# Kernel tuning notes

Measured on AMD Instinct MI355X. Metric: run time of the kernel, lower is better.

The kernel has to match this reference:

```python
import jax, jax.numpy as jnp
import numpy as np

EPS = 1e-5  # torch LayerNorm default

def _ln(x):
    # LayerNorm over last dim, no affine (elementwise_affine=False)
    m = jnp.mean(x, axis=-1, keepdims=True)
    v = jnp.var(x, axis=-1, keepdims=True)
    return (x - m) / jnp.sqrt(v + EPS)

def _build_orthogonal(phi):
    """Orthogonal matrix of the 'X' RBS circuit on d qubits (unary subspace).
    phi has 2d-3 angles: a descending diagonal of d-1 adjacent Givens rotations
    followed by an ascending diagonal of d-2. Each RBS(theta) acts on coords
    (k, k+1) as [[cos, sin], [-sin, cos]]."""
    d = (phi.shape[0] + 3) // 2
    W = jnp.eye(d, dtype=phi.dtype)
    wires = list(range(d - 1)) + list(range(d - 3, -1, -1))  # 2d-3 gates
    for g, k in enumerate(wires):
        c, s = jnp.cos(phi[g]), jnp.sin(phi[g])
        rk, rk1 = W[k], W[k + 1]
        W = W.at[k].set(c * rk + s * rk1)
        W = W.at[k + 1].set(-s * rk + c * rk1)
    return W

def setup_inputs() -> dict:
    key = jax.random.key(0)
    ks = jax.random.split(key, 8)
    B, N, E, H, dh = 16, 1024, 512, 8, 64
    return {
        "x": jax.random.normal(ks[0], (B, N, E), jnp.float32),
        "Wv": jax.random.normal(ks[1], (H, dh, dh), jnp.float32) / np.sqrt(dh).astype(np.float32),
        "bv": jnp.zeros((H, dh), jnp.float32),
        "phi": jax.random.uniform(ks[2], (H, 2 * dh - 3), jnp.float32, 0.0, 2.0 * np.pi),
        "W1": jax.random.normal(ks[3], (E, E), jnp.float32) / np.sqrt(E).astype(np.float32),
        "b1": jnp.zeros((E,), jnp.float32),
        "W2": jax.random.normal(ks[4], (E, E), jnp.float32) / np.sqrt(E).astype(np.float32),
        "b2": jnp.zeros((E,), jnp.float32),
    }

def reference(x, Wv, bv, phi, W1, b1, W2, b2):
    B, N, E = x.shape
    H = Wv.shape[0]
    dh = E // H
    xn = _ln(x)                                    # norm1
    xh = xn.reshape(B, N, H, dh)                   # per-head slices
    Worth = jax.vmap(_build_orthogonal)(phi)       # [H, dh, dh]
    # per-head value projection (nn.Linear weights stored as [in, out])
    V = jnp.einsum('bnhd,hde->bnhe', xh, Wv) + bv  # [B,N,H,dh]
    # quantum attention scores: loader(x_j) -> W(phi) -> inverse loader(x_i),
    # rescaled by |x_i||x_j|  ==  A_ij = x_i^T W(phi) x_j
    A = jnp.einsum('bnhd,hde,bmhe->bhnm', xh, Worth, xh)
    P = jax.nn.softmax(A / np.float32(np.sqrt(dh)), axis=-1)
    attn = jnp.einsum('bhnm,bmhe->bnhe', P, V)
    head_out = _ln(attn + xh)                      # per-head LN over dh
    res = head_out.reshape(B, N, E) + x            # MHA + residual
    # merger: Linear -> GELU(exact) -> Linear on norm2(res)
    h = jax.nn.gelu(_ln(res) @ W1 + b1, approximate=False) @ W2 + b2
    return h + res
```

## Files before the change

kernel.cpp:

```cpp
#include <hip/hip_runtime.h>
#include <hip/hip_bf16.h>
#include <math.h>

#define B_  16
#define N_  1024
#define E_  512
#define H_  8

typedef __attribute__((ext_vector_type(8)))  __bf16 bf16x8;
typedef __attribute__((ext_vector_type(4)))  float  f32x4;
typedef __attribute__((ext_vector_type(16))) float  f32x16;
typedef __attribute__((ext_vector_type(4)))  unsigned int u32x4;

struct alignas(16) bf8pack { __hip_bfloat16 v[8]; };
struct alignas(8)  bf4pack { __hip_bfloat16 v[4]; };

static __device__ __forceinline__ float bf2f(__hip_bfloat16 x) { return __bfloat162float(x); }
static __device__ __forceinline__ __hip_bfloat16 f2bf(float x) { return __float2bfloat16(x); }

static __device__ __forceinline__ unsigned pkbf(float lo, float hi) {
    unsigned r;
    asm("v_cvt_pk_bf16_f32 %0, %1, %2" : "=v"(r) : "v"(lo), "v"(hi));
    return r;
}
static __device__ __forceinline__ void swap32(unsigned &a, unsigned &b) {
    asm("v_permlane32_swap_b32 %0, %1" : "+v"(a), "+v"(b));
}
static __device__ __forceinline__ void gload16(const __hip_bfloat16* g, __hip_bfloat16* l) {
    __builtin_amdgcn_global_load_lds(
        (const __attribute__((address_space(1))) unsigned*)g,
        (__attribute__((address_space(3))) unsigned*)l, 16, 0, 0);
}
#define MFMA32(a, b, c) __builtin_amdgcn_mfma_f32_32x32x16_bf16((a), (b), (c), 0, 0, 0)
#define MFMA16(a, b, c) __builtin_amdgcn_mfma_f32_16x16x32_bf16((a), (b), (c), 0, 0, 0)

static __device__ __forceinline__ float gelu_f(float v) {
    float z = fabsf(v) * 0.70710678118654752f;
    float t = 1.0f / fmaf(0.3275911f, z, 1.0f);
    float p = t * fmaf(t, fmaf(t, fmaf(t, fmaf(t, 1.061405429f, -1.453152027f),
                                       1.421413741f), -0.284496736f), 0.254829592f);
    float e = __builtin_amdgcn_exp2f(-z * z * 1.4426950408889634f);
    float erf = 1.0f - p * e;
    erf = copysignf(erf, v);
    return 0.5f * v * (1.0f + erf);
}

__global__ __launch_bounds__(64) void k_worth(const float* __restrict__ phi,
                                              const float* __restrict__ Wv,
                                              __hip_bfloat16* __restrict__ worth_t,
                                              __hip_bfloat16* __restrict__ wvt) {
    const float SCL = 0.18033688011112042f;
    __shared__ float W[64 * 65];
    int h = blockIdx.x;
    int t = threadIdx.x;
    for (int i = 0; i < 64; ++i) W[i * 65 + t] = (i == t) ? 1.0f : 0.0f;
    for (int g = 0; g < 125; ++g) {
        int k = (g < 63) ? g : (124 - g);
        float ph = phi[h * 125 + g];
        float c = cosf(ph), s = sinf(ph);
        float a  = W[k * 65 + t];
        float b  = W[(k + 1) * 65 + t];
        W[k * 65 + t]       =  c * a + s * b;
        W[(k + 1) * 65 + t] = -s * a + c * b;
    }
    for (int d = 0; d < 64; ++d)
        worth_t[h * 4096 + t * 64 + d] = f2bf(W[d * 65 + t] * SCL);
    for (int d = 0; d < 64; ++d)
        wvt[h * 4096 + t * 64 + d] = f2bf(Wv[h * 4096 + d * 64 + t]);
}

__global__ __launch_bounds__(256) void k_transpose(const float* __restrict__ W1,
                                                   const float* __restrict__ W2,
                                                   __hip_bfloat16* __restrict__ w1t,
                                                   __hip_bfloat16* __restrict__ w2t) {
    const float* src = blockIdx.y ? W2 : W1;
    __hip_bfloat16* dst = blockIdx.y ? w2t : w1t;
    int i0 = (blockIdx.x & 7) * 64, o0 = (blockIdx.x >> 3) * 64;
    int tid = threadIdx.x;
    __shared__ float ts[64][65];
    int r = tid >> 4, c4 = (tid & 15) * 4;
#pragma unroll
    for (int j4 = 0; j4 < 4; ++j4) {
        float4 v = *reinterpret_cast<const float4*>(&src[(size_t)(i0 + r + 16 * j4) * 512 + o0 + c4]);
        ts[r + 16 * j4][c4 + 0] = v.x; ts[r + 16 * j4][c4 + 1] = v.y;
        ts[r + 16 * j4][c4 + 2] = v.z; ts[r + 16 * j4][c4 + 3] = v.w;
    }
    __syncthreads();
    int o = tid >> 3, cg = tid & 7;
#pragma unroll
    for (int half = 0; half < 2; ++half) {
        int oo = o + 32 * half;
        bf8pack p;
#pragma unroll
        for (int j = 0; j < 8; ++j) p.v[j] = f2bf(ts[cg * 8 + j][oo]);
        *reinterpret_cast<bf8pack*>(&dst[(size_t)(o0 + oo) * 512 + i0 + cg * 8]) = p;
    }
}

template <typename T>
__global__ __launch_bounds__(256) void k_ln(const T* __restrict__ in,
                                            __hip_bfloat16* __restrict__ out) {
    int w = threadIdx.x >> 6, l = threadIdx.x & 63;
    size_t row = (size_t)blockIdx.x * 4 + w;
    float vv[8];
    if constexpr (sizeof(T) == 4) {
        const float* p = (const float*)in + row * 512 + l * 8;
        float4 v0 = *reinterpret_cast<const float4*>(p);
        float4 v1 = *reinterpret_cast<const float4*>(p + 4);
        vv[0]=v0.x; vv[1]=v0.y; vv[2]=v0.z; vv[3]=v0.w;
        vv[4]=v1.x; vv[5]=v1.y; vv[6]=v1.z; vv[7]=v1.w;
    } else {
        const __hip_bfloat16* p = (const __hip_bfloat16*)in + row * 512 + l * 8;
        bf16x8 u = *reinterpret_cast<const bf16x8*>(p);
#pragma unroll
        for (int j = 0; j < 8; ++j) vv[j] = (float)u[j];
    }
    float s = 0.f, sq = 0.f;
#pragma unroll
    for (int j = 0; j < 8; ++j) { s += vv[j]; sq += vv[j] * vv[j]; }
#pragma unroll
    for (int o = 32; o >= 1; o >>= 1) { s += __shfl_xor(s, o); sq += __shfl_xor(sq, o); }
    float mean = s * (1.0f / 512.0f);
    float var  = sq * (1.0f / 512.0f) - mean * mean;
    float rstd = rsqrtf(var + 1e-5f);
    bf8pack ob;
#pragma unroll
    for (int j = 0; j < 8; ++j) ob.v[j] = f2bf((vv[j] - mean) * rstd);
    *reinterpret_cast<bf8pack*>(out + row * 512 + l * 8) = ob;
}

__global__ __launch_bounds__(256) void k_proj(const __hip_bfloat16* __restrict__ xn,
                                              const __hip_bfloat16* __restrict__ worth_t,
                                              const __hip_bfloat16* __restrict__ wvt,
                                              const float* __restrict__ bv,
                                              __hip_bfloat16* __restrict__ xw,
                                              __hip_bfloat16* __restrict__ vt) {
    int h = blockIdx.y, rt = blockIdx.x;
    int tid = threadIdx.x, w = tid >> 6, l = tid & 63;
    int lr = l & 15, lg = l >> 4;
    int nw = rt * 64 + w * 16;
    int b  = (rt * 64) >> 10;
    int n0 = (rt * 64) & 1023;
    size_t bh = (size_t)b * H_ + h;

    const __hip_bfloat16* xp = xn + (size_t)(nw + lr) * 512 + h * 64 + lg * 8;
    bf16x8 xf0 = *reinterpret_cast<const bf16x8*>(xp);
    bf16x8 xf1 = *reinterpret_cast<const bf16x8*>(xp + 32);

    f32x4 accw[4] = {}, accv[4] = {};
#pragma unroll
    for (int g = 0; g < 4; ++g) {
        const __hip_bfloat16* wp = worth_t + h * 4096 + (g * 16 + lr) * 64 + lg * 8;
        accw[g] = MFMA16(*reinterpret_cast<const bf16x8*>(wp), xf0, accw[g]);
        accw[g] = MFMA16(*reinterpret_cast<const bf16x8*>(wp + 32), xf1, accw[g]);
        const __hip_bfloat16* vp = wvt + h * 4096 + (g * 16 + lr) * 64 + lg * 8;
        accv[g] = MFMA16(xf0, *reinterpret_cast<const bf16x8*>(vp), accv[g]);
        accv[g] = MFMA16(xf1, *reinterpret_cast<const bf16x8*>(vp + 32), accv[g]);
    }
#pragma unroll
    for (int g = 0; g < 4; ++g) {
        bf4pack pw;
#pragma unroll
        for (int r = 0; r < 4; ++r) pw.v[r] = f2bf(accw[g][r]);
        *reinterpret_cast<bf4pack*>(xw + (bh * N_ + n0 + w * 16 + lr) * 64 + g * 16 + lg * 4) = pw;
        float bb = bv[h * 64 + g * 16 + lr];
        bf4pack pv;
#pragma unroll
        for (int r = 0; r < 4; ++r) pv.v[r] = f2bf(accv[g][r] + bb);
        *reinterpret_cast<bf4pack*>(vt + (bh * 64 + g * 16 + lr) * N_ + n0 + w * 16 + lg * 4) = pv;
    }
}

__global__ __launch_bounds__(512, 4) void k_attn(const __hip_bfloat16* __restrict__ xn,
                                                 const __hip_bfloat16* __restrict__ xw,
                                                 const __hip_bfloat16* __restrict__ vt,
                                                 const float* __restrict__ x,
                                                 __hip_bfloat16* __restrict__ res) {
    int h = blockIdx.x, b = blockIdx.z;
    int tid = threadIdx.x;
    int w = tid >> 6, l = tid & 63;
    int lq = l & 31, hi = l >> 5;
    int q0 = blockIdx.y * 256 + w * 32;
    size_t bh = (size_t)b * H_ + h;

    __shared__ __hip_bfloat16 kb[2][128 * 64];
    __shared__ __hip_bfloat16 vb[2][64 * 128];
    __shared__ float lred[8][32];

    int krow = w * 16 + (l >> 3);
    const __hip_bfloat16* ksrc = xn + ((size_t)b * N_ + krow) * 512 + h * 64
                               + (((l & 7) ^ (krow & 7)) << 3);
    int vrow0 = w * 8 + (l >> 4);
    int vrow1 = vrow0 + 4;
    const __hip_bfloat16* vsrc0 = vt + (bh * 64 + vrow0) * N_ + (((l & 15) ^ (vrow0 & 15)) << 3);
    const __hip_bfloat16* vsrc1 = vt + (bh * 64 + vrow1) * N_ + (((l & 15) ^ (vrow1 & 15)) << 3);

#define STAGE(t) do { int bf_ = (t) & 1; \
        gload16(ksrc + (size_t)((t) * 128) * 512,     &kb[bf_][(w * 16) * 64]); \
        gload16(ksrc + (size_t)((t) * 128 + 8) * 512, &kb[bf_][(w * 16 + 8) * 64]); \
        gload16(vsrc0 + (t) * 128, &vb[bf_][(w * 8) * 128]); \
        gload16(vsrc1 + (t) * 128, &vb[bf_][(w * 8 + 4) * 128]); } while (0)
#define TILE_BAR() do { \
        asm volatile("s_waitcnt vmcnt(0)" ::: "memory"); \
        __builtin_amdgcn_s_barrier(); \
        __builtin_amdgcn_sched_barrier(0); } while (0)

    const __hip_bfloat16* qp = xw + (bh * N_ + q0 + lq) * 64 + 8 * hi;
    bf16x8 qf0 = *reinterpret_cast<const bf16x8*>(qp);
    bf16x8 qf1 = *reinterpret_cast<const bf16x8*>(qp + 16);
    bf16x8 qf2 = *reinterpret_cast<const bf16x8*>(qp + 32);
    bf16x8 qf3 = *reinterpret_cast<const bf16x8*>(qp + 48);

    f32x16 o0 = {}, o1 = {};
    float l_run = 0.f;
    int kso = lq & 7;
    int vso = lq & 15;

    auto body = [&](int bf_, int mm) {
        const __hip_bfloat16* kc = &kb[bf_][mm * 64 * 64];
        const __hip_bfloat16* vc = &vb[bf_][0];
        f32x16 s0 = {}, s1 = {};
        __builtin_amdgcn_s_setprio(1);
#pragma unroll
        for (int kd = 0; kd < 4; ++kd) {
            bf16x8 qf = (kd == 0) ? qf0 : (kd == 1) ? qf1 : (kd == 2) ? qf2 : qf3;
            int sl = ((kd * 2 + hi) ^ kso) << 3;
            bf16x8 ka0 = *reinterpret_cast<const bf16x8*>(kc + lq * 64 + sl);
            bf16x8 ka1 = *reinterpret_cast<const bf16x8*>(kc + (lq + 32) * 64 + sl);
            s0 = MFMA32(ka0, qf, s0);
            s1 = MFMA32(ka1, qf, s1);
        }
        __builtin_amdgcn_s_setprio(0);
#pragma unroll
        for (int i = 0; i < 16; ++i) {
            s0[i] = __builtin_amdgcn_exp2f(s0[i]);
            s1[i] = __builtin_amdgcn_exp2f(s1[i]);
        }
        float ls = 0.f;
#pragma unroll
        for (int i = 0; i < 16; ++i) ls += s0[i] + s1[i];
        l_run += ls;
        bf16x8 pa[4];
        {
            unsigned u0 = pkbf(s0[0], s0[1]), u1 = pkbf(s0[2], s0[3]);
            unsigned u2 = pkbf(s0[4], s0[5]), u3 = pkbf(s0[6], s0[7]);
            swap32(u0, u2); swap32(u1, u3);
            u32x4 uu = {u0, u1, u2, u3};
            pa[0] = __builtin_bit_cast(bf16x8, uu);
        }
        {
            unsigned u0 = pkbf(s0[8], s0[9]),   u1 = pkbf(s0[10], s0[11]);
            unsigned u2 = pkbf(s0[12], s0[13]), u3 = pkbf(s0[14], s0[15]);
            swap32(u0, u2); swap32(u1, u3);
            u32x4 uu = {u0, u1, u2, u3};
            pa[1] = __builtin_bit_cast(bf16x8, uu);
        }
        {
            unsigned u0 = pkbf(s1[0], s1[1]), u1 = pkbf(s1[2], s1[3]);
            unsigned u2 = pkbf(s1[4], s1[5]), u3 = pkbf(s1[6], s1[7]);
            swap32(u0, u2); swap32(u1, u3);
            u32x4 uu = {u0, u1, u2, u3};
            pa[2] = __builtin_bit_cast(bf16x8, uu);
        }
        {
            unsigned u0 = pkbf(s1[8], s1[9]),   u1 = pkbf(s1[10], s1[11]);
            unsigned u2 = pkbf(s1[12], s1[13]), u3 = pkbf(s1[14], s1[15]);
            swap32(u0, u2); swap32(u1, u3);
            u32x4 uu = {u0, u1, u2, u3};
            pa[3] = __builtin_bit_cast(bf16x8, uu);
        }
        __builtin_amdgcn_s_setprio(1);
#pragma unroll
        for (int ks = 0; ks < 4; ++ks) {
            int sl = ((mm * 8 + ks * 2 + hi) ^ vso) << 3;
            bf16x8 v0 = *reinterpret_cast<const bf16x8*>(vc + lq * 128 + sl);
            bf16x8 v1 = *reinterpret_cast<const bf16x8*>(vc + (lq + 32) * 128 + sl);
            o0 = MFMA32(pa[ks], v0, o0);
            o1 = MFMA32(pa[ks], v1, o1);
        }
        __builtin_amdgcn_s_setprio(0);
    };

    STAGE(0);
    TILE_BAR();
    for (int t = 0; t < 7; ++t) {
        STAGE(t + 1);
        body(t & 1, 0);
        body(t & 1, 1);
        TILE_BAR();
    }
    body(1, 0);
    body(1, 1);

    float lt = l_run + __shfl_xor(l_run, 32);
    if (hi == 0) lred[w][lq] = 1.0f / lt;
#pragma unroll
    for (int r = 0; r < 16; ++r) {
        int qr = (r & 3) + 8 * (r >> 2) + 4 * hi;
        float li = lred[w][qr];
        size_t base = ((size_t)b * N_ + q0 + qr) * 512 + h * 64;
        float t0 = o0[r] * li + bf2f(xn[base + lq]);
        float t1 = o1[r] * li + bf2f(xn[base + 32 + lq]);
        float s1v = t0 + t1, s2v = t0 * t0 + t1 * t1;
#pragma unroll
        for (int off = 16; off >= 1; off >>= 1) { s1v += __shfl_xor(s1v, off); s2v += __shfl_xor(s2v, off); }
        float mean = s1v * (1.0f / 64.0f);
        float var  = s2v * (1.0f / 64.0f) - mean * mean;
        float rstd = rsqrtf(var + 1e-5f);
        res[base + lq]      = f2bf((t0 - mean) * rstd + x[base + lq]);
        res[base + 32 + lq] = f2bf((t1 - mean) * rstd + x[base + 32 + lq]);
    }
#undef STAGE
#undef TILE_BAR
}

template <int MODE>
__global__ __launch_bounds__(256, 5) void k_gemm(const __hip_bfloat16* __restrict__ A,
                                                 const __hip_bfloat16* __restrict__ Bt,
                                                 const float* __restrict__ bias,
                                                 const __hip_bfloat16* __restrict__ resid,
                                                 __hip_bfloat16* __restrict__ outb,
                                                 float* __restrict__ outf) {
    int m0 = blockIdx.x * 128, nn0 = blockIdx.y * 64;
    int tid = threadIdx.x, w = tid >> 6, l = tid & 63;
    int lr = l & 15, lg = l >> 4;
    __shared__ __hip_bfloat16 bs[2][64 * 128];

    int srow = w * 16 + (l >> 4);
    int sslot = l & 15;

#define GSTAGE(c) do { \
        _Pragma("unroll") \
        for (int i_ = 0; i_ < 4; ++i_) { \
            int row_ = srow + i_ * 4; \
            gload16(Bt + (size_t)(nn0 + row_) * 512 + (c) * 128 + ((sslot ^ (row_ & 15)) << 3), \
                    &bs[(c) & 1][(w * 16 + i_ * 4) * 128]); \
        } } while (0)

    GSTAGE(0);
    asm volatile("s_waitcnt vmcnt(0)" ::: "memory");
    __builtin_amdgcn_s_barrier();
    __builtin_amdgcn_sched_barrier(0);

    f32x4 acc0[4] = {}, acc1[4] = {};
    const __hip_bfloat16* ap0 = A + (size_t)(m0 + w * 32 + lr) * 512 + lg * 8;
    const __hip_bfloat16* ap1 = ap0 + 16 * 512;
#pragma unroll
    for (int c = 0; c < 4; ++c) {
        if (c < 3) GSTAGE(c + 1);
        const __hip_bfloat16* bc = &bs[c & 1][0];
#pragma unroll
        for (int kk = 0; kk < 4; ++kk) {
            bf16x8 a0 = *reinterpret_cast<const bf16x8*>(ap0 + c * 128 + kk * 32);
            bf16x8 a1 = *reinterpret_cast<const bf16x8*>(ap1 + c * 128 + kk * 32);
#pragma unroll
            for (int g = 0; g < 4; ++g) {
                int row = g * 16 + lr;
                bf16x8 bf = *reinterpret_cast<const bf16x8*>(
                    bc + row * 128 + (((kk * 4 + lg) ^ (row & 15)) << 3));
                acc0[g] = MFMA16(a0, bf, acc0[g]);
                acc1[g] = MFMA16(a1, bf, acc1[g]);
            }
        }
        if (c < 3) {
            asm volatile("s_waitcnt vmcnt(0)" ::: "memory");
            __builtin_amdgcn_s_barrier();
            __builtin_amdgcn_sched_barrier(0);
        }
    }
#undef GSTAGE
#pragma unroll
    for (int g = 0; g < 4; ++g) {
        int col = nn0 + g * 16 + lr;
        float bb = bias[col];
#pragma unroll
        for (int r = 0; r < 4; ++r) {
            int row0 = m0 + w * 32 + lg * 4 + r;
            float v0 = acc0[g][r] + bb;
            float v1 = acc1[g][r] + bb;
            if (MODE == 0) {
                outb[(size_t)row0 * 512 + col] = f2bf(gelu_f(v0));
                outb[(size_t)(row0 + 16) * 512 + col] = f2bf(gelu_f(v1));
            } else {
                size_t i0 = (size_t)row0 * 512 + col;
                size_t i1 = (size_t)(row0 + 16) * 512 + col;
                outf[i0] = v0 + bf2f(resid[i0]);
                outf[i1] = v1 + bf2f(resid[i1]);
            }
        }
    }
}

extern "C" void kernel_launch(void* const* d_in, const int* in_sizes, int n_in,
                              void* d_out, int out_size, void* d_ws, size_t ws_size,
                              hipStream_t stream) {
    const float* x   = (const float*)d_in[0];
    const float* Wv  = (const float*)d_in[1];
    const float* bv  = (const float*)d_in[2];
    const float* phi = (const float*)d_in[3];
    const float* W1  = (const float*)d_in[4];
    const float* b1  = (const float*)d_in[5];
    const float* W2  = (const float*)d_in[6];
    const float* b2  = (const float*)d_in[7];
    float* out = (float*)d_out;

    char* ws = (char*)d_ws;
    __hip_bfloat16* worth_t = (__hip_bfloat16*)(ws + 0);
    __hip_bfloat16* wvt     = (__hip_bfloat16*)(ws + 65536);
    __hip_bfloat16* w1t     = (__hip_bfloat16*)(ws + 131072);
    __hip_bfloat16* w2t     = (__hip_bfloat16*)(ws + 655360);
    __hip_bfloat16* xn      = (__hip_bfloat16*)(ws + 1179648);
    __hip_bfloat16* xw      = (__hip_bfloat16*)(ws + 17956864);
    __hip_bfloat16* vt      = (__hip_bfloat16*)(ws + 34734080);
    __hip_bfloat16* res     = (__hip_bfloat16*)(ws + 51511296);
    __hip_bfloat16* xn2     = (__hip_bfloat16*)(ws + 68288512);
    __hip_bfloat16* y1      = (__hip_bfloat16*)(ws + 85065728);

    k_worth<<<dim3(8), dim3(64), 0, stream>>>(phi, Wv, worth_t, wvt);
    k_transpose<<<dim3(64, 2), dim3(256), 0, stream>>>(W1, W2, w1t, w2t);
    k_ln<float><<<dim3(4096), dim3(256), 0, stream>>>(x, xn);
    k_proj<<<dim3(256, 8), dim3(256), 0, stream>>>(xn, worth_t, wvt, bv, xw, vt);
    k_attn<<<dim3(8, 4, 16), dim3(512), 0, stream>>>(xn, xw, vt, x, res);
    k_ln<__hip_bfloat16><<<dim3(4096), dim3(256), 0, stream>>>(res, xn2);
    k_gemm<0><<<dim3(128, 8), dim3(256), 0, stream>>>(xn2, w1t, b1, nullptr, y1, nullptr);
    k_gemm<1><<<dim3(128, 8), dim3(256), 0, stream>>>(y1, w2t, b2, res, nullptr, out);
}
```

Measured before the change: 179.4 us.

## Software-pipeline attention over 64-key tiles, merge prep kernels, read bf16 residual

Attention now processes 64-key tiles with a triple-buffered K and quad-buffered V ring. QK^T of the next tile overlaps with PV of the previous tile, and the barrier waits with vmcnt(2) so loads stay in flight. The two weight-prep kernels are merged into one launch, which saves a launch. The first LayerNorm also writes a bf16 copy of x so attention reads a half-size residual instead of fp32. That copy costs extra writes and adds bf16 rounding to the residual, and more LDS use may limit occupancy.

```diff
diff --git a/kernel.cpp b/kernel.cpp
--- a/kernel.cpp
+++ b/kernel.cpp
@@ -45,61 +45,67 @@
     return 0.5f * v * (1.0f + erf);
 }
 
-__global__ __launch_bounds__(64) void k_worth(const float* __restrict__ phi,
+__global__ __launch_bounds__(256) void k_prep(const float* __restrict__ phi,
                                               const float* __restrict__ Wv,
+                                              const float* __restrict__ W1,
+                                              const float* __restrict__ W2,
                                               __hip_bfloat16* __restrict__ worth_t,
-                                              __hip_bfloat16* __restrict__ wvt) {
-    const float SCL = 0.18033688011112042f;
-    __shared__ float W[64 * 65];
-    int h = blockIdx.x;
-    int t = threadIdx.x;
-    for (int i = 0; i < 64; ++i) W[i * 65 + t] = (i == t) ? 1.0f : 0.0f;
-    for (int g = 0; g < 125; ++g) {
-        int k = (g < 63) ? g : (124 - g);
-        float ph = phi[h * 125 + g];
-        float c = cosf(ph), s = sinf(ph);
-        float a  = W[k * 65 + t];
-        float b  = W[(k + 1) * 65 + t];
-        W[k * 65 + t]       =  c * a + s * b;
-        W[(k + 1) * 65 + t] = -s * a + c * b;
-    }
-    for (int d = 0; d < 64; ++d)
-        worth_t[h * 4096 + t * 64 + d] = f2bf(W[d * 65 + t] * SCL);
-    for (int d = 0; d < 64; ++d)
-        wvt[h * 4096 + t * 64 + d] = f2bf(Wv[h * 4096 + d * 64 + t]);
-}
-
-__global__ __launch_bounds__(256) void k_transpose(const float* __restrict__ W1,
-                                                   const float* __restrict__ W2,
-                                                   __hip_bfloat16* __restrict__ w1t,
-                                                   __hip_bfloat16* __restrict__ w2t) {
-    const float* src = blockIdx.y ? W2 : W1;
-    __hip_bfloat16* dst = blockIdx.y ? w2t : w1t;
-    int i0 = (blockIdx.x & 7) * 64, o0 = (blockIdx.x >> 3) * 64;
+                                              __hip_bfloat16* __restrict__ wvt,
+                                              __hip_bfloat16* __restrict__ w1t,
+                                              __hip_bfloat16* __restrict__ w2t) {
+    __shared__ float sh[64 * 65];
     int tid = threadIdx.x;
-    __shared__ float ts[64][65];
-    int r = tid >> 4, c4 = (tid & 15) * 4;
-#pragma unroll
-    for (int j4 = 0; j4 < 4; ++j4) {
-        float4 v = *reinterpret_cast<const float4*>(&src[(size_t)(i0 + r + 16 * j4) * 512 + o0 + c4]);
-        ts[r + 16 * j4][c4 + 0] = v.x; ts[r + 16 * j4][c4 + 1] = v.y;
-        ts[r + 16 * j4][c4 + 2] = v.z; ts[r + 16 * j4][c4 + 3] = v.w;
-    }
-    __syncthreads();
-    int o = tid >> 3, cg = tid & 7;
-#pragma unroll
-    for (int half = 0; half < 2; ++half) {
-        int oo = o + 32 * half;
-        bf8pack p;
-#pragma unroll
-        for (int j = 0; j < 8; ++j) p.v[j] = f2bf(ts[cg * 8 + j][oo]);
-        *reinterpret_cast<bf8pack*>(&dst[(size_t)(o0 + oo) * 512 + i0 + cg * 8]) = p;
-    }
-}
-
-template <typename T>
+    if (blockIdx.x < 128) {
+        int bid = blockIdx.x;
+        const float* src = (bid & 1) ? W2 : W1;
+        __hip_bfloat16* dst = (bid & 1) ? w2t : w1t;
+        int tile = bid >> 1;
+        int i0 = (tile & 7) * 64, o0 = (tile >> 3) * 64;
+        float (*ts)[65] = (float(*)[65])sh;
+        int r = tid >> 4, c4 = (tid & 15) * 4;
+#pragma unroll
+        for (int j4 = 0; j4 < 4; ++j4) {
+            float4 v = *reinterpret_cast<const float4*>(&src[(size_t)(i0 + r + 16 * j4) * 512 + o0 + c4]);
+            ts[r + 16 * j4][c4 + 0] = v.x; ts[r + 16 * j4][c4 + 1] = v.y;
+            ts[r + 16 * j4][c4 + 2] = v.z; ts[r + 16 * j4][c4 + 3] = v.w;
+        }
+        __syncthreads();
+        int o = tid >> 3, cg = tid & 7;
+#pragma unroll
+        for (int half = 0; half < 2; ++half) {
+            int oo = o + 32 * half;
+            bf8pack p;
+#pragma unroll
+            for (int j = 0; j < 8; ++j) p.v[j] = f2bf(ts[cg * 8 + j][oo]);
+            *reinterpret_cast<bf8pack*>(&dst[(size_t)(o0 + oo) * 512 + i0 + cg * 8]) = p;
+        }
+    } else {
+        const float SCL = 0.18033688011112042f;
+        int h = blockIdx.x - 128;
+        int t = tid;
+        if (t < 64) {
+            for (int i = 0; i < 64; ++i) sh[i * 65 + t] = (i == t) ? 1.0f : 0.0f;
+            for (int g = 0; g < 125; ++g) {
+                int k = (g < 63) ? g : (124 - g);
+                float ph = phi[h * 125 + g];
+                float c = cosf(ph), s = sinf(ph);
+                float a  = sh[k * 65 + t];
+                float b  = sh[(k + 1) * 65 + t];
+                sh[k * 65 + t]       =  c * a + s * b;
+                sh[(k + 1) * 65 + t] = -s * a + c * b;
+            }
+            for (int d = 0; d < 64; ++d)
+                worth_t[h * 4096 + t * 64 + d] = f2bf(sh[d * 65 + t] * SCL);
+            for (int d = 0; d < 64; ++d)
+                wvt[h * 4096 + t * 64 + d] = f2bf(Wv[h * 4096 + d * 64 + t]);
+        }
+    }
+}
+
+template <typename T, bool WX>
 __global__ __launch_bounds__(256) void k_ln(const T* __restrict__ in,
-                                            __hip_bfloat16* __restrict__ out) {
+                                            __hip_bfloat16* __restrict__ out,
+                                            __hip_bfloat16* __restrict__ outx) {
     int w = threadIdx.x >> 6, l = threadIdx.x & 63;
     size_t row = (size_t)blockIdx.x * 4 + w;
     float vv[8];
@@ -114,6 +120,12 @@
         bf16x8 u = *reinterpret_cast<const bf16x8*>(p);
 #pragma unroll
         for (int j = 0; j < 8; ++j) vv[j] = (float)u[j];
+    }
+    if constexpr (WX) {
+        bf8pack xo;
+#pragma unroll
+        for (int j = 0; j < 8; ++j) xo.v[j] = f2bf(vv[j]);
+        *reinterpret_cast<bf8pack*>(outx + row * 512 + l * 8) = xo;
     }
     float s = 0.f, sq = 0.f;
 #pragma unroll
@@ -174,34 +186,30 @@
 __global__ __launch_bounds__(512, 4) void k_attn(const __hip_bfloat16* __restrict__ xn,
                                                  const __hip_bfloat16* __restrict__ xw,
                                                  const __hip_bfloat16* __restrict__ vt,
-                                                 const float* __restrict__ x,
+                                                 const __hip_bfloat16* __restrict__ xb,
                                                  __hip_bfloat16* __restrict__ res) {
     int h = blockIdx.x, b = blockIdx.z;
     int tid = threadIdx.x;
     int w = tid >> 6, l = tid & 63;
     int lq = l & 31, hi = l >> 5;
+    int so = lq & 7;
     int q0 = blockIdx.y * 256 + w * 32;
     size_t bh = (size_t)b * H_ + h;
 
-    __shared__ __hip_bfloat16 kb[2][128 * 64];
-    __shared__ __hip_bfloat16 vb[2][64 * 128];
+    __shared__ __hip_bfloat16 kb[3][4096];
+    __shared__ __hip_bfloat16 vb[4][4096];
     __shared__ float lred[8][32];
 
-    int krow = w * 16 + (l >> 3);
-    const __hip_bfloat16* ksrc = xn + ((size_t)b * N_ + krow) * 512 + h * 64
-                               + (((l & 7) ^ (krow & 7)) << 3);
-    int vrow0 = w * 8 + (l >> 4);
-    int vrow1 = vrow0 + 4;
-    const __hip_bfloat16* vsrc0 = vt + (bh * 64 + vrow0) * N_ + (((l & 15) ^ (vrow0 & 15)) << 3);
-    const __hip_bfloat16* vsrc1 = vt + (bh * 64 + vrow1) * N_ + (((l & 15) ^ (vrow1 & 15)) << 3);
-
-#define STAGE(t) do { int bf_ = (t) & 1; \
-        gload16(ksrc + (size_t)((t) * 128) * 512,     &kb[bf_][(w * 16) * 64]); \
-        gload16(ksrc + (size_t)((t) * 128 + 8) * 512, &kb[bf_][(w * 16 + 8) * 64]); \
-        gload16(vsrc0 + (t) * 128, &vb[bf_][(w * 8) * 128]); \
-        gload16(vsrc1 + (t) * 128, &vb[bf_][(w * 8 + 4) * 128]); } while (0)
-#define TILE_BAR() do { \
-        asm volatile("s_waitcnt vmcnt(0)" ::: "memory"); \
+    int rloc = w * 8 + (l >> 3);
+    int gs = ((l & 7) ^ (rloc & 7)) << 3;
+    const __hip_bfloat16* ksrc = xn + ((size_t)b * N_ + rloc) * 512 + h * 64 + gs;
+    const __hip_bfloat16* vsrc = vt + (bh * 64 + rloc) * N_ + gs;
+
+#define STAGE(t) do { \
+        gload16(ksrc + (size_t)(t) * 64 * 512, &kb[(t) % 3][w * 512]); \
+        gload16(vsrc + (t) * 64, &vb[(t) & 3][w * 512]); } while (0)
+#define TILE_BAR(nvm) do { \
+        asm volatile("s_waitcnt vmcnt(" #nvm ")" ::: "memory"); \
         __builtin_amdgcn_s_barrier(); \
         __builtin_amdgcn_sched_barrier(0); } while (0)
 
@@ -213,24 +221,38 @@
 
     f32x16 o0 = {}, o1 = {};
     float l_run = 0.f;
-    int kso = lq & 7;
-    int vso = lq & 15;
-
-    auto body = [&](int bf_, int mm) {
-        const __hip_bfloat16* kc = &kb[bf_][mm * 64 * 64];
-        const __hip_bfloat16* vc = &vb[bf_][0];
-        f32x16 s0 = {}, s1 = {};
+    f32x16 s0, s1;
+    bf16x8 paA[4], paB[4];
+
+    auto qk = [&](int t) {
+        const __hip_bfloat16* kc = &kb[t % 3][0];
+        s0 = (f32x16){}; s1 = (f32x16){};
         __builtin_amdgcn_s_setprio(1);
 #pragma unroll
         for (int kd = 0; kd < 4; ++kd) {
             bf16x8 qf = (kd == 0) ? qf0 : (kd == 1) ? qf1 : (kd == 2) ? qf2 : qf3;
-            int sl = ((kd * 2 + hi) ^ kso) << 3;
+            int sl = ((kd * 2 + hi) ^ so) << 3;
             bf16x8 ka0 = *reinterpret_cast<const bf16x8*>(kc + lq * 64 + sl);
             bf16x8 ka1 = *reinterpret_cast<const bf16x8*>(kc + (lq + 32) * 64 + sl);
             s0 = MFMA32(ka0, qf, s0);
             s1 = MFMA32(ka1, qf, s1);
         }
         __builtin_amdgcn_s_setprio(0);
+    };
+    auto pv = [&](int t, const bf16x8* pa) {
+        const __hip_bfloat16* vc = &vb[t & 3][0];
+        __builtin_amdgcn_s_setprio(1);
+#pragma unroll
+        for (int ks = 0; ks < 4; ++ks) {
+            int sl = ((ks * 2 + hi) ^ so) << 3;
+            bf16x8 v0 = *reinterpret_cast<const bf16x8*>(vc + lq * 64 + sl);
+            bf16x8 v1 = *reinterpret_cast<const bf16x8*>(vc + (lq + 32) * 64 + sl);
+            o0 = MFMA32(pa[ks], v0, o0);
+            o1 = MFMA32(pa[ks], v1, o1);
+        }
+        __builtin_amdgcn_s_setprio(0);
+    };
+    auto exppack = [&](bf16x8* pa) {
 #pragma unroll
         for (int i = 0; i < 16; ++i) {
             s0[i] = __builtin_amdgcn_exp2f(s0[i]);
@@ -240,7 +262,6 @@
 #pragma unroll
         for (int i = 0; i < 16; ++i) ls += s0[i] + s1[i];
         l_run += ls;
-        bf16x8 pa[4];
         {
             unsigned u0 = pkbf(s0[0], s0[1]), u1 = pkbf(s0[2], s0[3]);
             unsigned u2 = pkbf(s0[4], s0[5]), u3 = pkbf(s0[6], s0[7]);
@@ -269,28 +290,34 @@
             u32x4 uu = {u0, u1, u2, u3};
             pa[3] = __builtin_bit_cast(bf16x8, uu);
         }
-        __builtin_amdgcn_s_setprio(1);
-#pragma unroll
-        for (int ks = 0; ks < 4; ++ks) {
-            int sl = ((mm * 8 + ks * 2 + hi) ^ vso) << 3;
-            bf16x8 v0 = *reinterpret_cast<const bf16x8*>(vc + lq * 128 + sl);
-            bf16x8 v1 = *reinterpret_cast<const bf16x8*>(vc + (lq + 32) * 128 + sl);
-            o0 = MFMA32(pa[ks], v0, o0);
-            o1 = MFMA32(pa[ks], v1, o1);
-        }
-        __builtin_amdgcn_s_setprio(0);
     };
 
-    STAGE(0);
-    TILE_BAR();
-    for (int t = 0; t < 7; ++t) {
-        STAGE(t + 1);
-        body(t & 1, 0);
-        body(t & 1, 1);
-        TILE_BAR();
-    }
-    body(1, 0);
-    body(1, 1);
+    STAGE(0); STAGE(1);
+    TILE_BAR(2);
+    STAGE(2);
+    qk(0); exppack(paA);
+    TILE_BAR(2);
+
+    for (int tp = 0; tp < 6; ++tp) {
+        int t = 2 * tp + 1;
+        STAGE(t + 2);
+        qk(t);
+        pv(t - 1, paA);
+        exppack(paB);
+        TILE_BAR(2);
+        STAGE(t + 3);
+        qk(t + 1);
+        pv(t, paB);
+        exppack(paA);
+        TILE_BAR(2);
+    }
+    STAGE(15);
+    qk(13); pv(12, paA); exppack(paB);
+    TILE_BAR(2);
+    qk(14); pv(13, paB); exppack(paA);
+    TILE_BAR(0);
+    qk(15); pv(14, paA); exppack(paB);
+    pv(15, paB);
 
     float lt = l_run + __shfl_xor(l_run, 32);
     if (hi == 0) lred[w][lq] = 1.0f / lt;
@@ -307,8 +334,8 @@
         float mean = s1v * (1.0f / 64.0f);
         float var  = s2v * (1.0f / 64.0f) - mean * mean;
         float rstd = rsqrtf(var + 1e-5f);
-        res[base + lq]      = f2bf((t0 - mean) * rstd + x[base + lq]);
-        res[base + 32 + lq] = f2bf((t1 - mean) * rstd + x[base + 32 + lq]);
+        res[base + lq]      = f2bf((t0 - mean) * rstd + bf2f(xb[base + lq]));
+        res[base + 32 + lq] = f2bf((t1 - mean) * rstd + bf2f(xb[base + 32 + lq]));
     }
 #undef STAGE
 #undef TILE_BAR
@@ -415,13 +442,13 @@
     __hip_bfloat16* res     = (__hip_bfloat16*)(ws + 51511296);
     __hip_bfloat16* xn2     = (__hip_bfloat16*)(ws + 68288512);
     __hip_bfloat16* y1      = (__hip_bfloat16*)(ws + 85065728);
-
-    k_worth<<<dim3(8), dim3(64), 0, stream>>>(phi, Wv, worth_t, wvt);
-    k_transpose<<<dim3(64, 2), dim3(256), 0, stream>>>(W1, W2, w1t, w2t);
-    k_ln<float><<<dim3(4096), dim3(256), 0, stream>>>(x, xn);
+    __hip_bfloat16* xb      = (__hip_bfloat16*)(ws + 101842944);
+
+    k_prep<<<dim3(136), dim3(256), 0, stream>>>(phi, Wv, W1, W2, worth_t, wvt, w1t, w2t);
+    k_ln<float, true><<<dim3(4096), dim3(256), 0, stream>>>(x, xn, xb);
     k_proj<<<dim3(256, 8), dim3(256), 0, stream>>>(xn, worth_t, wvt, bv, xw, vt);
-    k_attn<<<dim3(8, 4, 16), dim3(512), 0, stream>>>(xn, xw, vt, x, res);
-    k_ln<__hip_bfloat16><<<dim3(4096), dim3(256), 0, stream>>>(res, xn2);
+    k_attn<<<dim3(8, 4, 16), dim3(512), 0, stream>>>(xn, xw, vt, xb, res);
+    k_ln<__hip_bfloat16, false><<<dim3(4096), dim3(256), 0, stream>>>(res, xn2, nullptr);
     k_gemm<0><<<dim3(128, 8), dim3(256), 0, stream>>>(xn2, w1t, b1, nullptr, y1, nullptr);
     k_gemm<1><<<dim3(128, 8), dim3(256), 0, stream>>>(y1, w2t, b2, res, nullptr, out);
 }
```

After: 186.0 us. 1.04x slower.

## Fold LayerNorm2 into GEMM1 epilogue via row stats and weight column sums

Applied to the files above, without the earlier changes.

Replaces the second LayerNorm kernel, which wrote a normalized bf16 copy of res, with a small row-statistics kernel. GEMM1 now runs directly on res and applies rstd*(acc) - mean*rstd*colsum(W1) + b1 in its epilogue. It also merges the weight prep kernels into one launch, stages the proj outputs through LDS for coalesced stores, and passes a bf16 copy of x to attention instead of fp32. The cost is precision: GEMM1 multiplies un-centered bf16 res values, while the column sums are fp32 over the unrounded W1 rather than the bf16 w1t the GEMM uses, so the mean correction no longer cancels exactly.

```diff
diff --git a/kernel.cpp b/kernel.cpp
--- a/kernel.cpp
+++ b/kernel.cpp
@@ -45,76 +45,82 @@
     return 0.5f * v * (1.0f + erf);
 }
 
-__global__ __launch_bounds__(64) void k_worth(const float* __restrict__ phi,
+__global__ __launch_bounds__(256) void k_prep(const float* __restrict__ phi,
                                               const float* __restrict__ Wv,
+                                              const float* __restrict__ W1,
+                                              const float* __restrict__ W2,
                                               __hip_bfloat16* __restrict__ worth_t,
-                                              __hip_bfloat16* __restrict__ wvt) {
-    const float SCL = 0.18033688011112042f;
-    __shared__ float W[64 * 65];
-    int h = blockIdx.x;
-    int t = threadIdx.x;
-    for (int i = 0; i < 64; ++i) W[i * 65 + t] = (i == t) ? 1.0f : 0.0f;
-    for (int g = 0; g < 125; ++g) {
-        int k = (g < 63) ? g : (124 - g);
-        float ph = phi[h * 125 + g];
-        float c = cosf(ph), s = sinf(ph);
-        float a  = W[k * 65 + t];
-        float b  = W[(k + 1) * 65 + t];
-        W[k * 65 + t]       =  c * a + s * b;
-        W[(k + 1) * 65 + t] = -s * a + c * b;
-    }
-    for (int d = 0; d < 64; ++d)
-        worth_t[h * 4096 + t * 64 + d] = f2bf(W[d * 65 + t] * SCL);
-    for (int d = 0; d < 64; ++d)
-        wvt[h * 4096 + t * 64 + d] = f2bf(Wv[h * 4096 + d * 64 + t]);
-}
-
-__global__ __launch_bounds__(256) void k_transpose(const float* __restrict__ W1,
-                                                   const float* __restrict__ W2,
-                                                   __hip_bfloat16* __restrict__ w1t,
-                                                   __hip_bfloat16* __restrict__ w2t) {
-    const float* src = blockIdx.y ? W2 : W1;
-    __hip_bfloat16* dst = blockIdx.y ? w2t : w1t;
-    int i0 = (blockIdx.x & 7) * 64, o0 = (blockIdx.x >> 3) * 64;
+                                              __hip_bfloat16* __restrict__ wvt,
+                                              __hip_bfloat16* __restrict__ w1t,
+                                              __hip_bfloat16* __restrict__ w2t,
+                                              float* __restrict__ csum1) {
+    __shared__ float sh[64 * 65];
     int tid = threadIdx.x;
-    __shared__ float ts[64][65];
-    int r = tid >> 4, c4 = (tid & 15) * 4;
-#pragma unroll
-    for (int j4 = 0; j4 < 4; ++j4) {
-        float4 v = *reinterpret_cast<const float4*>(&src[(size_t)(i0 + r + 16 * j4) * 512 + o0 + c4]);
-        ts[r + 16 * j4][c4 + 0] = v.x; ts[r + 16 * j4][c4 + 1] = v.y;
-        ts[r + 16 * j4][c4 + 2] = v.z; ts[r + 16 * j4][c4 + 3] = v.w;
-    }
-    __syncthreads();
-    int o = tid >> 3, cg = tid & 7;
-#pragma unroll
-    for (int half = 0; half < 2; ++half) {
-        int oo = o + 32 * half;
-        bf8pack p;
-#pragma unroll
-        for (int j = 0; j < 8; ++j) p.v[j] = f2bf(ts[cg * 8 + j][oo]);
-        *reinterpret_cast<bf8pack*>(&dst[(size_t)(o0 + oo) * 512 + i0 + cg * 8]) = p;
-    }
-}
-
-template <typename T>
-__global__ __launch_bounds__(256) void k_ln(const T* __restrict__ in,
-                                            __hip_bfloat16* __restrict__ out) {
+    if (blockIdx.x < 128) {
+        int bid = blockIdx.x;
+        const float* src = (bid & 1) ? W2 : W1;
+        __hip_bfloat16* dst = (bid & 1) ? w2t : w1t;
+        int tile = bid >> 1;
+        int i0 = (tile & 7) * 64, o0 = (tile >> 3) * 64;
+        float (*ts)[65] = (float(*)[65])sh;
+        int r = tid >> 4, c4 = (tid & 15) * 4;
+#pragma unroll
+        for (int j4 = 0; j4 < 4; ++j4) {
+            float4 v = *reinterpret_cast<const float4*>(&src[(size_t)(i0 + r + 16 * j4) * 512 + o0 + c4]);
+            ts[r + 16 * j4][c4 + 0] = v.x; ts[r + 16 * j4][c4 + 1] = v.y;
+            ts[r + 16 * j4][c4 + 2] = v.z; ts[r + 16 * j4][c4 + 3] = v.w;
+        }
+        __syncthreads();
+        int o = tid >> 3, cg = tid & 7;
+#pragma unroll
+        for (int half = 0; half < 2; ++half) {
+            int oo = o + 32 * half;
+            bf8pack p;
+#pragma unroll
+            for (int j = 0; j < 8; ++j) p.v[j] = f2bf(ts[cg * 8 + j][oo]);
+            *reinterpret_cast<bf8pack*>(&dst[(size_t)(o0 + oo) * 512 + i0 + cg * 8]) = p;
+        }
+    } else if (blockIdx.x < 136) {
+        const float SCL = 0.18033688011112042f;
+        int h = blockIdx.x - 128;
+        int t = tid;
+        if (t < 64) {
+            for (int i = 0; i < 64; ++i) sh[i * 65 + t] = (i == t) ? 1.0f : 0.0f;
+            for (int g = 0; g < 125; ++g) {
+                int k = (g < 63) ? g : (124 - g);
+                float ph = phi[h * 125 + g];
+                float c = cosf(ph), s = sinf(ph);
+                float a  = sh[k * 65 + t];
+                float b  = sh[(k + 1) * 65 + t];
+                sh[k * 65 + t]       =  c * a + s * b;
+                sh[(k + 1) * 65 + t] = -s * a + c * b;
+            }
+            for (int d = 0; d < 64; ++d)
+                worth_t[h * 4096 + t * 64 + d] = f2bf(sh[d * 65 + t] * SCL);
+            for (int d = 0; d < 64; ++d)
+                wvt[h * 4096 + t * 64 + d] = f2bf(Wv[h * 4096 + d * 64 + t]);
+        }
+    } else {
+        int o = (blockIdx.x - 136) * 256 + tid;
+        float s = 0.f;
+        for (int i = 0; i < 512; ++i) s += W1[(size_t)i * 512 + o];
+        csum1[o] = s;
+    }
+}
+
+__global__ __launch_bounds__(256) void k_ln1(const float* __restrict__ in,
+                                             __hip_bfloat16* __restrict__ out,
+                                             __hip_bfloat16* __restrict__ outx) {
     int w = threadIdx.x >> 6, l = threadIdx.x & 63;
     size_t row = (size_t)blockIdx.x * 4 + w;
-    float vv[8];
-    if constexpr (sizeof(T) == 4) {
-        const float* p = (const float*)in + row * 512 + l * 8;
-        float4 v0 = *reinterpret_cast<const float4*>(p);
-        float4 v1 = *reinterpret_cast<const float4*>(p + 4);
-        vv[0]=v0.x; vv[1]=v0.y; vv[2]=v0.z; vv[3]=v0.w;
-        vv[4]=v1.x; vv[5]=v1.y; vv[6]=v1.z; vv[7]=v1.w;
-    } else {
-        const __hip_bfloat16* p = (const __hip_bfloat16*)in + row * 512 + l * 8;
-        bf16x8 u = *reinterpret_cast<const bf16x8*>(p);
-#pragma unroll
-        for (int j = 0; j < 8; ++j) vv[j] = (float)u[j];
-    }
+    const float* p = in + row * 512 + l * 8;
+    float4 v0 = *reinterpret_cast<const float4*>(p);
+    float4 v1 = *reinterpret_cast<const float4*>(p + 4);
+    float vv[8] = {v0.x, v0.y, v0.z, v0.w, v1.x, v1.y, v1.z, v1.w};
+    bf8pack xo;
+#pragma unroll
+    for (int j = 0; j < 8; ++j) xo.v[j] = f2bf(vv[j]);
+    *reinterpret_cast<bf8pack*>(outx + row * 512 + l * 8) = xo;
     float s = 0.f, sq = 0.f;
 #pragma unroll
     for (int j = 0; j < 8; ++j) { s += vv[j]; sq += vv[j] * vv[j]; }
@@ -127,6 +133,22 @@
 #pragma unroll
     for (int j = 0; j < 8; ++j) ob.v[j] = f2bf((vv[j] - mean) * rstd);
     *reinterpret_cast<bf8pack*>(out + row * 512 + l * 8) = ob;
+}
+
+__global__ __launch_bounds__(256) void k_rowstat(const __hip_bfloat16* __restrict__ res,
+                                                 float2* __restrict__ rs) {
+    int w = threadIdx.x >> 6, l = threadIdx.x & 63;
+    size_t row = (size_t)blockIdx.x * 4 + w;
+    bf16x8 u = *reinterpret_cast<const bf16x8*>(res + row * 512 + l * 8);
+    float s = 0.f, sq = 0.f;
+#pragma unroll
+    for (int j = 0; j < 8; ++j) { float a = (float)u[j]; s += a; sq = fmaf(a, a, sq); }
+#pragma unroll
+    for (int o = 32; o >= 1; o >>= 1) { s += __shfl_xor(s, o); sq += __shfl_xor(sq, o); }
+    float mean = s * (1.0f / 512.0f);
+    float var  = sq * (1.0f / 512.0f) - mean * mean;
+    float rstd = rsqrtf(var + 1e-5f);
+    if (l == 0) rs[row] = make_float2(rstd, mean * rstd);
 }
 
 __global__ __launch_bounds__(256) void k_proj(const __hip_bfloat16* __restrict__ xn,
@@ -143,6 +165,9 @@
     int n0 = (rt * 64) & 1023;
     size_t bh = (size_t)b * H_ + h;
 
+    __shared__ __hip_bfloat16 xw_l[64 * 72];
+    __shared__ __hip_bfloat16 vt_l[64 * 72];
+
     const __hip_bfloat16* xp = xn + (size_t)(nw + lr) * 512 + h * 64 + lg * 8;
     bf16x8 xf0 = *reinterpret_cast<const bf16x8*>(xp);
     bf16x8 xf1 = *reinterpret_cast<const bf16x8*>(xp + 32);
@@ -162,19 +187,33 @@
         bf4pack pw;
 #pragma unroll
         for (int r = 0; r < 4; ++r) pw.v[r] = f2bf(accw[g][r]);
-        *reinterpret_cast<bf4pack*>(xw + (bh * N_ + n0 + w * 16 + lr) * 64 + g * 16 + lg * 4) = pw;
+        *reinterpret_cast<bf4pack*>(&xw_l[(w * 16 + lr) * 72 + g * 16 + lg * 4]) = pw;
         float bb = bv[h * 64 + g * 16 + lr];
         bf4pack pv;
 #pragma unroll
         for (int r = 0; r < 4; ++r) pv.v[r] = f2bf(accv[g][r] + bb);
-        *reinterpret_cast<bf4pack*>(vt + (bh * 64 + g * 16 + lr) * N_ + n0 + w * 16 + lg * 4) = pv;
+        *reinterpret_cast<bf4pack*>(&vt_l[(g * 16 + lr) * 72 + w * 16 + lg * 4]) = pv;
+    }
+    __syncthreads();
+    {
+        int rr = tid >> 2, c0 = (tid & 3) * 16;
+        bf8pack p0 = *reinterpret_cast<const bf8pack*>(&xw_l[rr * 72 + c0]);
+        bf8pack p1 = *reinterpret_cast<const bf8pack*>(&xw_l[rr * 72 + c0 + 8]);
+        __hip_bfloat16* d1 = xw + (bh * N_ + n0 + rr) * 64 + c0;
+        *reinterpret_cast<bf8pack*>(d1)     = p0;
+        *reinterpret_cast<bf8pack*>(d1 + 8) = p1;
+        bf8pack q0 = *reinterpret_cast<const bf8pack*>(&vt_l[rr * 72 + c0]);
+        bf8pack q1 = *reinterpret_cast<const bf8pack*>(&vt_l[rr * 72 + c0 + 8]);
+        __hip_bfloat16* d2 = vt + (bh * 64 + rr) * N_ + n0 + c0;
+        *reinterpret_cast<bf8pack*>(d2)     = q0;
+        *reinterpret_cast<bf8pack*>(d2 + 8) = q1;
     }
 }
 
 __global__ __launch_bounds__(512, 4) void k_attn(const __hip_bfloat16* __restrict__ xn,
                                                  const __hip_bfloat16* __restrict__ xw,
                                                  const __hip_bfloat16* __restrict__ vt,
-                                                 const float* __restrict__ x,
+                                                 const __hip_bfloat16* __restrict__ xb,
                                                  __hip_bfloat16* __restrict__ res) {
     int h = blockIdx.x, b = blockIdx.z;
     int tid = threadIdx.x;
@@ -307,8 +346,8 @@
         float mean = s1v * (1.0f / 64.0f);
         float var  = s2v * (1.0f / 64.0f) - mean * mean;
         float rstd = rsqrtf(var + 1e-5f);
-        res[base + lq]      = f2bf((t0 - mean) * rstd + x[base + lq]);
-        res[base + 32 + lq] = f2bf((t1 - mean) * rstd + x[base + 32 + lq]);
+        res[base + lq]      = f2bf((t0 - mean) * rstd + bf2f(xb[base + lq]));
+        res[base + 32 + lq] = f2bf((t1 - mean) * rstd + bf2f(xb[base + 32 + lq]));
     }
 #undef STAGE
 #undef TILE_BAR
@@ -319,6 +358,8 @@
                                                  const __hip_bfloat16* __restrict__ Bt,
                                                  const float* __restrict__ bias,
                                                  const __hip_bfloat16* __restrict__ resid,
+                                                 const float2* __restrict__ rstat,
+                                                 const float* __restrict__ csum,
                                                  __hip_bfloat16* __restrict__ outb,
                                                  float* __restrict__ outf) {
     int m0 = blockIdx.x * 128, nn0 = blockIdx.y * 64;
@@ -369,23 +410,32 @@
         }
     }
 #undef GSTAGE
+    float2 rsA[4], rsB[4];
+    if (MODE == 0) {
+#pragma unroll
+        for (int r = 0; r < 4; ++r) {
+            rsA[r] = rstat[m0 + w * 32 + lg * 4 + r];
+            rsB[r] = rstat[m0 + w * 32 + lg * 4 + r + 16];
+        }
+    }
 #pragma unroll
     for (int g = 0; g < 4; ++g) {
         int col = nn0 + g * 16 + lr;
         float bb = bias[col];
+        float cc = (MODE == 0) ? csum[col] : 0.f;
 #pragma unroll
         for (int r = 0; r < 4; ++r) {
             int row0 = m0 + w * 32 + lg * 4 + r;
-            float v0 = acc0[g][r] + bb;
-            float v1 = acc1[g][r] + bb;
             if (MODE == 0) {
+                float v0 = fmaf(acc0[g][r], rsA[r].x, fmaf(-rsA[r].y, cc, bb));
+                float v1 = fmaf(acc1[g][r], rsB[r].x, fmaf(-rsB[r].y, cc, bb));
                 outb[(size_t)row0 * 512 + col] = f2bf(gelu_f(v0));
                 outb[(size_t)(row0 + 16) * 512 + col] = f2bf(gelu_f(v1));
             } else {
                 size_t i0 = (size_t)row0 * 512 + col;
                 size_t i1 = (size_t)(row0 + 16) * 512 + col;
-                outf[i0] = v0 + bf2f(resid[i0]);
-                outf[i1] = v1 + bf2f(resid[i1]);
+                outf[i0] = acc0[g][r] + bb + bf2f(resid[i0]);
+                outf[i1] = acc1[g][r] + bb + bf2f(resid[i1]);
             }
         }
     }
@@ -409,19 +459,20 @@
     __hip_bfloat16* wvt     = (__hip_bfloat16*)(ws + 65536);
     __hip_bfloat16* w1t     = (__hip_bfloat16*)(ws + 131072);
     __hip_bfloat16* w2t     = (__hip_bfloat16*)(ws + 655360);
-    __hip_bfloat16* xn      = (__hip_bfloat16*)(ws + 1179648);
-    __hip_bfloat16* xw      = (__hip_bfloat16*)(ws + 17956864);
-    __hip_bfloat16* vt      = (__hip_bfloat16*)(ws + 34734080);
-    __hip_bfloat16* res     = (__hip_bfloat16*)(ws + 51511296);
-    __hip_bfloat16* xn2     = (__hip_bfloat16*)(ws + 68288512);
-    __hip_bfloat16* y1      = (__hip_bfloat16*)(ws + 85065728);
-
-    k_worth<<<dim3(8), dim3(64), 0, stream>>>(phi, Wv, worth_t, wvt);
-    k_transpose<<<dim3(64, 2), dim3(256), 0, stream>>>(W1, W2, w1t, w2t);
-    k_ln<float><<<dim3(4096), dim3(256), 0, stream>>>(x, xn);
+    float*          csum1   = (float*)(ws + 1179648);
+    float2*         rstat   = (float2*)(ws + 1181696);
+    __hip_bfloat16* xn      = (__hip_bfloat16*)(ws + 1312768);
+    __hip_bfloat16* xw      = (__hip_bfloat16*)(ws + 18089984);
+    __hip_bfloat16* vt      = (__hip_bfloat16*)(ws + 34867200);
+    __hip_bfloat16* res     = (__hip_bfloat16*)(ws + 51644416);
+    __hip_bfloat16* y1      = (__hip_bfloat16*)(ws + 68421632);
+    __hip_bfloat16* xb      = (__hip_bfloat16*)(ws + 85198848);
+
+    k_prep<<<dim3(138), dim3(256), 0, stream>>>(phi, Wv, W1, W2, worth_t, wvt, w1t, w2t, csum1);
+    k_ln1<<<dim3(4096), dim3(256), 0, stream>>>(x, xn, xb);
     k_proj<<<dim3(256, 8), dim3(256), 0, stream>>>(xn, worth_t, wvt, bv, xw, vt);
-    k_attn<<<dim3(8, 4, 16), dim3(512), 0, stream>>>(xn, xw, vt, x, res);
-    k_ln<__hip_bfloat16><<<dim3(4096), dim3(256), 0, stream>>>(res, xn2);
-    k_gemm<0><<<dim3(128, 8), dim3(256), 0, stream>>>(xn2, w1t, b1, nullptr, y1, nullptr);
-    k_gemm<1><<<dim3(128, 8), dim3(256), 0, stream>>>(y1, w2t, b2, res, nullptr, out);
-}
+    k_attn<<<dim3(8, 4, 16), dim3(512), 0, stream>>>(xn, xw, vt, xb, res);
+    k_rowstat<<<dim3(4096), dim3(256), 0, stream>>>(res, rstat);
+    k_gemm<0><<<dim3(128, 8), dim3(256), 0, stream>>>(res, w1t, b1, nullptr, rstat, csum1, y1, nullptr);
+    k_gemm<1><<<dim3(128, 8), dim3(256), 0, stream>>>(y1, w2t, b2, res, nullptr, nullptr, nullptr, out);
+}
```

Result: no change. 178.3 us (-0.6%).
